# Kernel tuning notes

Hardware: AMD Instinct MI355X
Metric: run time of the kernel (lower is better)

Reference implementation:

```python
import jax, jax.numpy as jnp
import numpy as np

N = 100000      # nodes
E = 1200000     # edges (avg degree ~12)
D_IN = 64
D_OUT = 64


def setup_inputs() -> dict:
    key = jax.random.key(0)
    k1, k2, k3, k4 = jax.random.split(key, 4)
    x = jax.random.normal(k1, (N, D_IN), dtype=jnp.float32)
    # learned params (glorot-ish init)
    W = jax.random.normal(k2, (D_IN, D_OUT), dtype=jnp.float32) / np.sqrt(D_IN).astype(np.float32)
    b = jnp.zeros((D_OUT,), dtype=jnp.float32)
    src = jax.random.randint(k3, (E,), 0, N, dtype=jnp.int32)
    dst = jax.random.randint(k4, (E,), 0, N, dtype=jnp.int32)
    return {"x": x, "W": W, "b": b, "src": src, "dst": dst}


def reference(x, W, b, src, dst):
    # GCN layer: h = relu( D^-1/2 A D^-1/2 (x @ W) + b ), dropout=0 (eval)
    ones = jnp.ones(src.shape[0], dtype=x.dtype)
    deg_out = jax.ops.segment_sum(ones, src, num_segments=N)   # out-degree of source nodes
    deg_in = jax.ops.segment_sum(ones, dst, num_segments=N)    # in-degree of dest nodes
    norm_src = jax.lax.rsqrt(jnp.maximum(deg_out, 1.0))
    norm_dst = jax.lax.rsqrt(jnp.maximum(deg_in, 1.0))

    h = x @ W                                                  # [N, D_OUT] dense transform
    msg = h[src] * norm_src[src][:, None]                      # [E, D_OUT] gathered, pre-normalized messages
    agg = jax.ops.segment_sum(msg, dst, num_segments=N)        # [N, D_OUT] sparse aggregation
    out = agg * norm_dst[:, None] + b
    return jax.nn.relu(out)
```

## Files before the change

### kernel.cpp

```cpp
#include <hip/hip_runtime.h>
#include <hip/hip_bf16.h>

#define N_NODES 100000
#define N_EDGES 1200000
#define DCH 64

#define NT 512

#define SB 192
#define SCHUNK (N_EDGES / SB)

#define HB 96
#define CHUNK (N_EDGES / HB)
#define HALF_BINS 50000
#define HALF_WORDS 12500

#define GEMMB 384
#define GWAVES (GEMMB * NT / 64)


#define BNODES 256
#define KBUK ((N_NODES + BNODES - 1) / BNODES)
#define CAPE 6144

#define OFF_DEG      0
#define OFF_GCUR     100096
#define OFF_FLAG     101760
#define OFF_ESORT    102144
#define OFF_HS       9711616

__device__ __forceinline__ float load_f(const void* p, int i, int f32) {
    if (f32) return ((const float*)p)[i];
    return __bfloat162float(((const __hip_bfloat16*)p)[i]);
}

__device__ __forceinline__ unsigned short f2bf_bits(float f) {
    __hip_bfloat16 h = __float2bfloat16(f);
    return __builtin_bit_cast(unsigned short, h);
}

__global__ __launch_bounds__(NT, 6)
void fused_kernel(const int* __restrict__ src,
                  const int* __restrict__ dst,
                  const void* __restrict__ x,
                  const void* __restrict__ W,
                  unsigned int* __restrict__ deg_packed,
                  int* __restrict__ gcur,
                  unsigned int* __restrict__ esort,
                  int* __restrict__ flag,
                  __hip_bfloat16* __restrict__ hs) {
    __shared__ unsigned int h[HALF_WORDS];
    int tid = threadIdx.x;
    int bid = blockIdx.x;

    if (bid < SB) {
        int* cnt  = (int*)h;
        int* base = cnt + KBUK;
        int* cur  = base + KBUK;
        for (int i = tid; i < KBUK; i += NT) { cnt[i] = 0; cur[i] = 0; }
        __syncthreads();
        int e0 = bid * SCHUNK;
        const int2* src2 = (const int2*)(src + e0);
        const int2* dst2 = (const int2*)(dst + e0);
        int npair = SCHUNK >> 1;
        for (int p = tid; p < npair; p += NT) {
            int2 dp = dst2[p];
            atomicAdd(&cnt[dp.x >> 8], 1);
            atomicAdd(&cnt[dp.y >> 8], 1);
        }
        __syncthreads();
        for (int i = tid; i < KBUK; i += NT)
            base[i] = atomicAdd(&gcur[i], cnt[i]);
        __syncthreads();
        for (int p = tid; p < npair; p += NT) {
            int2 sp = src2[p];
            int2 dp = dst2[p];
            int b0 = dp.x >> 8, b1 = dp.y >> 8;
            int pos0 = base[b0] + atomicAdd(&cur[b0], 1);
            if (pos0 < CAPE)
                esort[b0 * CAPE + pos0] =
                    (unsigned int)sp.x | ((unsigned int)(dp.x & 255) << 24);
            int pos1 = base[b1] + atomicAdd(&cur[b1], 1);
            if (pos1 < CAPE)
                esort[b1 * CAPE + pos1] =
                    (unsigned int)sp.y | ((unsigned int)(dp.y & 255) << 24);
        }
        if (bid == 0) {
            __syncthreads();
            if (tid == 0) cnt[0] = 0;
            __syncthreads();
            if (tid < 256) {
                const unsigned short* u = (const unsigned short*)x;
                int c = 0;
                for (int i = tid * 16; i < tid * 16 + 16; ++i) {
                    unsigned short v = u[2 * i];
                    int e = (v >> 7) & 0xFF;
                    if (e >= 141) c++;
                }
                if (c) atomicAdd(&cnt[0], c);
            }
            __syncthreads();
            if (tid == 0) *flag = (cnt[0] > 256) ? 1 : 0;
        }
    } else if (bid < SB + 2 * HB) {
        int hb = bid - SB;
        int c = hb >> 1, half = hb & 1;
        for (int w = tid; w < HALF_WORDS; w += NT) h[w] = 0;
        __syncthreads();
        int lo = half * HALF_BINS;
        int e0 = c * CHUNK;
        const int2* src2 = (const int2*)(src + e0);
        int npair = CHUNK >> 1;
        for (int p = tid; p < npair; p += NT) {
            int2 sp = src2[p];
            int n0 = sp.x - lo, n1 = sp.y - lo;
            if ((unsigned)n0 < (unsigned)HALF_BINS)
                atomicAdd(&h[n0 >> 2], 1u << ((n0 & 3) * 8));
            if ((unsigned)n1 < (unsigned)HALF_BINS)
                atomicAdd(&h[n1 >> 2], 1u << ((n1 & 3) * 8));
        }
        __syncthreads();
        unsigned int* dp = deg_packed + half * HALF_WORDS;
        for (int w = tid; w < HALF_WORDS; w += NT) {
            unsigned int v = h[w];
            if (v) atomicAdd(&dp[w], v);
        }
    } else {
        int* sn = (int*)h;
        if (tid == 0) sn[0] = 0;
        __syncthreads();
        if (tid < 256) {
            const unsigned short* u = (const unsigned short*)x;
            int c = 0;
            for (int i = tid * 16; i < tid * 16 + 16; ++i) {
                unsigned short v = u[2 * i];
                int e = (v >> 7) & 0xFF;
                if (e >= 141) c++;
            }
            if (c) atomicAdd(sn, c);
        }
        __syncthreads();
        int f32 = sn[0] > 256;
        __syncthreads();

        float* wt = (float*)h;
        for (int i = tid; i < DCH * DCH; i += NT) {
            int kk = i >> 6, cc = i & 63;
            wt[cc * 68 + kk] = load_f(W, i, f32);
        }
        __syncthreads();

        int lane = tid & 63;
        const float4* wrow = (const float4*)(wt + lane * 68);
        float4 wq0 = wrow[0],  wq1 = wrow[1],  wq2 = wrow[2],  wq3 = wrow[3];
        float4 wq4 = wrow[4],  wq5 = wrow[5],  wq6 = wrow[6],  wq7 = wrow[7];
        float4 wq8 = wrow[8],  wq9 = wrow[9],  wq10 = wrow[10], wq11 = wrow[11];
        float4 wq12 = wrow[12], wq13 = wrow[13], wq14 = wrow[14], wq15 = wrow[15];

        int wave = ((bid - (SB + 2 * HB)) * NT + tid) >> 6;
#define RLA(i) __int_as_float(__builtin_amdgcn_readlane(xiA, (i)))
#define RLB(i) __int_as_float(__builtin_amdgcn_readlane(xiB, (i)))
#define GRP(j, V) \
    a0 = fmaf(RLA(4*(j)+0), (V).x, a0); a1 = fmaf(RLA(4*(j)+1), (V).y, a1); \
    a2 = fmaf(RLA(4*(j)+2), (V).z, a2); a3 = fmaf(RLA(4*(j)+3), (V).w, a3); \
    c0 = fmaf(RLB(4*(j)+0), (V).x, c0); c1 = fmaf(RLB(4*(j)+1), (V).y, c1); \
    c2 = fmaf(RLB(4*(j)+2), (V).z, c2); c3 = fmaf(RLB(4*(j)+3), (V).w, c3);

        for (int node = wave; node < N_NODES; node += 2 * GWAVES) {
            int nodeB = node + GWAVES;
            int hasB = nodeB < N_NODES;
            float xvA = load_f(x, node * DCH + lane, f32);
            float xvB = hasB ? load_f(x, nodeB * DCH + lane, f32) : 0.0f;
            int xiA = __float_as_int(xvA);
            int xiB = __float_as_int(xvB);
            float a0 = 0.f, a1 = 0.f, a2 = 0.f, a3 = 0.f;
            float c0 = 0.f, c1 = 0.f, c2 = 0.f, c3 = 0.f;
            GRP(0, wq0)   GRP(1, wq1)   GRP(2, wq2)   GRP(3, wq3)
            GRP(4, wq4)   GRP(5, wq5)   GRP(6, wq6)   GRP(7, wq7)
            GRP(8, wq8)   GRP(9, wq9)   GRP(10, wq10) GRP(11, wq11)
            GRP(12, wq12) GRP(13, wq13) GRP(14, wq14) GRP(15, wq15)
            hs[node * DCH + lane] = __float2bfloat16((a0 + a1) + (a2 + a3));
            if (hasB)
                hs[nodeB * DCH + lane] = __float2bfloat16((c0 + c1) + (c2 + c3));
        }
#undef RLA
#undef RLB
#undef GRP
    }
}

__global__ __launch_bounds__(1024)
void sortgather_kernel(const __hip_bfloat16* __restrict__ hs,
                       const unsigned int* __restrict__ esort,
                       const int* __restrict__ gcur,
                       const unsigned int* __restrict__ deg_packed,
                       const void* __restrict__ b,
                       const int* __restrict__ flag,
                       void* __restrict__ out) {
    __shared__ unsigned int ebuf[CAPE];
    __shared__ int cnt[BNODES];
    __shared__ int loc[BNODES];
    __shared__ int sc[BNODES];
    __shared__ int cur[BNODES];
    __shared__ float tab[256];
    int k = blockIdx.x, tid = threadIdx.x;
    int bbase = k * CAPE;
    int m = gcur[k];
    if (m > CAPE) m = CAPE;

    if (tid < BNODES) { cnt[tid] = 0; cur[tid] = 0; }
    if (tid < 256) tab[tid] = rsqrtf(fmaxf((float)tid, 1.0f));
    __syncthreads();
    for (int e = tid; e < m; e += 1024)
        atomicAdd(&cnt[esort[bbase + e] >> 24], 1);
    __syncthreads();
    int v = 0;
    if (tid < BNODES) { v = cnt[tid]; sc[tid] = v; }
    __syncthreads();
    for (int off = 1; off < BNODES; off <<= 1) {
        int add = 0;
        if (tid < BNODES && tid >= off) add = sc[tid - off];
        __syncthreads();
        if (tid < BNODES) sc[tid] += add;
        __syncthreads();
    }
    if (tid < BNODES) loc[tid] = sc[tid] - v;
    __syncthreads();
    for (int e = tid; e < m; e += 1024) {
        unsigned int w = esort[bbase + e];
        int r = w >> 24;
        unsigned int s = w & 0xFFFFFFu;
        unsigned int dw = deg_packed[s >> 2];
        unsigned int degb = (dw >> ((s & 3) * 8)) & 0xFFu;
        int pos = loc[r] + atomicAdd(&cur[r], 1);
        ebuf[pos] = s | (degb << 24);
    }
    __syncthreads();

    int f32 = *flag;
    int lane = tid & 63, wv = tid >> 6;
    int q = lane >> 4;
    int cg = lane & 15;
    const unsigned short* hsu = (const unsigned short*)hs;
    float b0 = load_f(b, cg * 4 + 0, f32);
    float b1 = load_f(b, cg * 4 + 1, f32);
    float b2 = load_f(b, cg * 4 + 2, f32);
    float b3 = load_f(b, cg * 4 + 3, f32);
    int nlo = k * BNODES;
    for (int base = wv; base < BNODES; base += 32) {
        int tA = base, tB = base + 16;
        int nodeA = nlo + tA, nodeB = nlo + tB;
        int begA = loc[tA], degA = cnt[tA];
        int begB = loc[tB], degB = cnt[tB];
        float4 aA0 = {0.f,0.f,0.f,0.f}, aA1 = {0.f,0.f,0.f,0.f};
        float4 aB0 = {0.f,0.f,0.f,0.f}, aB1 = {0.f,0.f,0.f,0.f};
        int dmax = degA > degB ? degA : degB;
        for (int j0 = 0; j0 < dmax; j0 += 8) {
            int i0 = j0 + q, i1 = j0 + 4 + q;
            unsigned int wA0 = ebuf[(i0 < degA) ? (begA + i0) : 0];
            unsigned int wA1 = ebuf[(i1 < degA) ? (begA + i1) : 0];
            unsigned int wB0 = ebuf[(i0 < degB) ? (begB + i0) : 0];
            unsigned int wB1 = ebuf[(i1 < degB) ? (begB + i1) : 0];
            unsigned int sA0 = wA0 & 0xFFFFFFu, sA1 = wA1 & 0xFFFFFFu;
            unsigned int sB0 = wB0 & 0xFFFFFFu, sB1 = wB1 & 0xFFFFFFu;
            float fA0 = tab[wA0 >> 24], fA1 = tab[wA1 >> 24];
            float fB0 = tab[wB0 >> 24], fB1 = tab[wB1 >> 24];
            uint2 uA0 = ((const uint2*)(hsu + sA0 * DCH))[cg];
            uint2 uA1 = ((const uint2*)(hsu + sA1 * DCH))[cg];
            uint2 uB0 = ((const uint2*)(hsu + sB0 * DCH))[cg];
            uint2 uB1 = ((const uint2*)(hsu + sB1 * DCH))[cg];
            if (i0 < degA) {
                aA0.x = fmaf(__uint_as_float(uA0.x << 16),        fA0, aA0.x);
                aA0.y = fmaf(__uint_as_float(uA0.x & 0xFFFF0000u), fA0, aA0.y);
                aA0.z = fmaf(__uint_as_float(uA0.y << 16),        fA0, aA0.z);
                aA0.w = fmaf(__uint_as_float(uA0.y & 0xFFFF0000u), fA0, aA0.w);
            }
            if (i1 < degA) {
                aA1.x = fmaf(__uint_as_float(uA1.x << 16),        fA1, aA1.x);
                aA1.y = fmaf(__uint_as_float(uA1.x & 0xFFFF0000u), fA1, aA1.y);
                aA1.z = fmaf(__uint_as_float(uA1.y << 16),        fA1, aA1.z);
                aA1.w = fmaf(__uint_as_float(uA1.y & 0xFFFF0000u), fA1, aA1.w);
            }
            if (i0 < degB) {
                aB0.x = fmaf(__uint_as_float(uB0.x << 16),        fB0, aB0.x);
                aB0.y = fmaf(__uint_as_float(uB0.x & 0xFFFF0000u), fB0, aB0.y);
                aB0.z = fmaf(__uint_as_float(uB0.y << 16),        fB0, aB0.z);
                aB0.w = fmaf(__uint_as_float(uB0.y & 0xFFFF0000u), fB0, aB0.w);
            }
            if (i1 < degB) {
                aB1.x = fmaf(__uint_as_float(uB1.x << 16),        fB1, aB1.x);
                aB1.y = fmaf(__uint_as_float(uB1.x & 0xFFFF0000u), fB1, aB1.y);
                aB1.z = fmaf(__uint_as_float(uB1.y << 16),        fB1, aB1.z);
                aB1.w = fmaf(__uint_as_float(uB1.y & 0xFFFF0000u), fB1, aB1.w);
            }
        }
        float4 oA, oB;
        oA.x = aA0.x + aA1.x; oA.y = aA0.y + aA1.y;
        oA.z = aA0.z + aA1.z; oA.w = aA0.w + aA1.w;
        oB.x = aB0.x + aB1.x; oB.y = aB0.y + aB1.y;
        oB.z = aB0.z + aB1.z; oB.w = aB0.w + aB1.w;
        oA.x += __shfl_xor(oA.x, 16); oA.y += __shfl_xor(oA.y, 16);
        oA.z += __shfl_xor(oA.z, 16); oA.w += __shfl_xor(oA.w, 16);
        oA.x += __shfl_xor(oA.x, 32); oA.y += __shfl_xor(oA.y, 32);
        oA.z += __shfl_xor(oA.z, 32); oA.w += __shfl_xor(oA.w, 32);
        oB.x += __shfl_xor(oB.x, 16); oB.y += __shfl_xor(oB.y, 16);
        oB.z += __shfl_xor(oB.z, 16); oB.w += __shfl_xor(oB.w, 16);
        oB.x += __shfl_xor(oB.x, 32); oB.y += __shfl_xor(oB.y, 32);
        oB.z += __shfl_xor(oB.z, 32); oB.w += __shfl_xor(oB.w, 32);
        int myNode = (lane < 16) ? nodeA : nodeB;
        int myDeg  = (lane < 16) ? degA : degB;
        float4 o   = (lane < 16) ? oA : oB;
        if (lane < 32 && myNode < N_NODES) {
            float nrm = rsqrtf(fmaxf((float)myDeg, 1.0f));
            o.x = fmaxf(o.x * nrm + b0, 0.0f);
            o.y = fmaxf(o.y * nrm + b1, 0.0f);
            o.z = fmaxf(o.z * nrm + b2, 0.0f);
            o.w = fmaxf(o.w * nrm + b3, 0.0f);
            if (f32) {
                ((float4*)out)[myNode * 16 + cg] = o;
            } else {
                ushort4 s;
                s.x = f2bf_bits(o.x);
                s.y = f2bf_bits(o.y);
                s.z = f2bf_bits(o.z);
                s.w = f2bf_bits(o.w);
                ((ushort4*)out)[myNode * 16 + cg] = s;
            }
        }
    }
}

extern "C" void kernel_launch(void* const* d_in, const int* in_sizes, int n_in,
                              void* d_out, int out_size, void* d_ws, size_t ws_size,
                              hipStream_t stream) {
    const void* x   = d_in[0];
    const void* W   = d_in[1];
    const void* b   = d_in[2];
    const int*  src = (const int*)d_in[3];
    const int*  dst = (const int*)d_in[4];

    char* ws = (char*)d_ws;
    unsigned int* deg_packed = (unsigned int*)(ws + OFF_DEG);
    int* gcur     = (int*)(ws + OFF_GCUR);
    int* flag     = (int*)(ws + OFF_FLAG);
    unsigned int* esort = (unsigned int*)(ws + OFF_ESORT);
    __hip_bfloat16* hs  = (__hip_bfloat16*)(ws + OFF_HS);

    (void)hipMemsetAsync(ws, 0, OFF_FLAG + 4, stream);

    fused_kernel<<<SB + 2 * HB + GEMMB, NT, 0, stream>>>(
        src, dst, x, W, deg_packed, gcur, esort, flag, hs);

    sortgather_kernel<<<KBUK, 1024, 0, stream>>>(
        hs, esort, gcur, deg_packed, b, flag, d_out);
}
```

Baseline: 183.9 us.

## Make every fused block do GEMM, degree histogram and bucketing in sequence

The fused kernel drops its role-specialised block ranges (scatter, histogram, GEMM). Each of 256 blocks of 1024 threads now runs a share of the dense transform, then a two-pass packed source-degree histogram over its own edge chunk, then the destination bucketing. Buckets shrink from 256 to 128 nodes, so the sort/gather kernel gets about twice as many blocks at 512 threads each. The aim is better load balance and more gather-phase parallelism. The cost is that each block now runs all phases one after another, with extra barriers and two LDS histogram passes per block.

```diff
diff --git a/kernel.cpp b/kernel.cpp
--- a/kernel.cpp
+++ b/kernel.cpp
@@ -5,29 +5,25 @@
 #define N_EDGES 1200000
 #define DCH 64
 
-#define NT 512
-
-#define SB 192
-#define SCHUNK (N_EDGES / SB)
-
-#define HB 96
-#define CHUNK (N_EDGES / HB)
+#define FB 256
+#define NT 1024
+#define EPB 4688
+#define GW_TOT (FB * NT / 64)
+
 #define HALF_BINS 50000
 #define HALF_WORDS 12500
 
-#define GEMMB 384
-#define GWAVES (GEMMB * NT / 64)
-
-
-#define BNODES 256
+#define BNODES 128
 #define KBUK ((N_NODES + BNODES - 1) / BNODES)
-#define CAPE 6144
+#define CAPE 3008
+
+#define NT2 512
 
 #define OFF_DEG      0
 #define OFF_GCUR     100096
-#define OFF_FLAG     101760
-#define OFF_ESORT    102144
-#define OFF_HS       9711616
+#define OFF_FLAG     103296
+#define OFF_ESORT    103424
+#define OFF_HS       9512704
 
 __device__ __forceinline__ float load_f(const void* p, int i, int f32) {
     if (f32) return ((const float*)p)[i];
@@ -39,7 +35,7 @@
     return __builtin_bit_cast(unsigned short, h);
 }
 
-__global__ __launch_bounds__(NT, 6)
+__global__ __launch_bounds__(NT, 4)
 void fused_kernel(const int* __restrict__ src,
                   const int* __restrict__ dst,
                   const void* __restrict__ x,
@@ -53,96 +49,25 @@
     int tid = threadIdx.x;
     int bid = blockIdx.x;
 
-    if (bid < SB) {
-        int* cnt  = (int*)h;
-        int* base = cnt + KBUK;
-        int* cur  = base + KBUK;
-        for (int i = tid; i < KBUK; i += NT) { cnt[i] = 0; cur[i] = 0; }
-        __syncthreads();
-        int e0 = bid * SCHUNK;
-        const int2* src2 = (const int2*)(src + e0);
-        const int2* dst2 = (const int2*)(dst + e0);
-        int npair = SCHUNK >> 1;
-        for (int p = tid; p < npair; p += NT) {
-            int2 dp = dst2[p];
-            atomicAdd(&cnt[dp.x >> 8], 1);
-            atomicAdd(&cnt[dp.y >> 8], 1);
-        }
-        __syncthreads();
-        for (int i = tid; i < KBUK; i += NT)
-            base[i] = atomicAdd(&gcur[i], cnt[i]);
-        __syncthreads();
-        for (int p = tid; p < npair; p += NT) {
-            int2 sp = src2[p];
-            int2 dp = dst2[p];
-            int b0 = dp.x >> 8, b1 = dp.y >> 8;
-            int pos0 = base[b0] + atomicAdd(&cur[b0], 1);
-            if (pos0 < CAPE)
-                esort[b0 * CAPE + pos0] =
-                    (unsigned int)sp.x | ((unsigned int)(dp.x & 255) << 24);
-            int pos1 = base[b1] + atomicAdd(&cur[b1], 1);
-            if (pos1 < CAPE)
-                esort[b1 * CAPE + pos1] =
-                    (unsigned int)sp.y | ((unsigned int)(dp.y & 255) << 24);
-        }
-        if (bid == 0) {
-            __syncthreads();
-            if (tid == 0) cnt[0] = 0;
-            __syncthreads();
-            if (tid < 256) {
-                const unsigned short* u = (const unsigned short*)x;
-                int c = 0;
-                for (int i = tid * 16; i < tid * 16 + 16; ++i) {
-                    unsigned short v = u[2 * i];
-                    int e = (v >> 7) & 0xFF;
-                    if (e >= 141) c++;
-                }
-                if (c) atomicAdd(&cnt[0], c);
-            }
-            __syncthreads();
-            if (tid == 0) *flag = (cnt[0] > 256) ? 1 : 0;
-        }
-    } else if (bid < SB + 2 * HB) {
-        int hb = bid - SB;
-        int c = hb >> 1, half = hb & 1;
-        for (int w = tid; w < HALF_WORDS; w += NT) h[w] = 0;
-        __syncthreads();
-        int lo = half * HALF_BINS;
-        int e0 = c * CHUNK;
-        const int2* src2 = (const int2*)(src + e0);
-        int npair = CHUNK >> 1;
-        for (int p = tid; p < npair; p += NT) {
-            int2 sp = src2[p];
-            int n0 = sp.x - lo, n1 = sp.y - lo;
-            if ((unsigned)n0 < (unsigned)HALF_BINS)
-                atomicAdd(&h[n0 >> 2], 1u << ((n0 & 3) * 8));
-            if ((unsigned)n1 < (unsigned)HALF_BINS)
-                atomicAdd(&h[n1 >> 2], 1u << ((n1 & 3) * 8));
-        }
-        __syncthreads();
-        unsigned int* dp = deg_packed + half * HALF_WORDS;
-        for (int w = tid; w < HALF_WORDS; w += NT) {
-            unsigned int v = h[w];
-            if (v) atomicAdd(&dp[w], v);
-        }
-    } else {
-        int* sn = (int*)h;
-        if (tid == 0) sn[0] = 0;
-        __syncthreads();
-        if (tid < 256) {
-            const unsigned short* u = (const unsigned short*)x;
-            int c = 0;
-            for (int i = tid * 16; i < tid * 16 + 16; ++i) {
-                unsigned short v = u[2 * i];
-                int e = (v >> 7) & 0xFF;
-                if (e >= 141) c++;
-            }
-            if (c) atomicAdd(sn, c);
-        }
-        __syncthreads();
-        int f32 = sn[0] > 256;
-        __syncthreads();
-
+    int* sn = (int*)h;
+    if (tid == 0) sn[0] = 0;
+    __syncthreads();
+    if (tid < 256) {
+        const unsigned short* u = (const unsigned short*)x;
+        int c = 0;
+        for (int i = tid * 16; i < tid * 16 + 16; ++i) {
+            unsigned short v = u[2 * i];
+            int e = (v >> 7) & 0xFF;
+            if (e >= 141) c++;
+        }
+        if (c) atomicAdd(sn, c);
+    }
+    __syncthreads();
+    int f32 = sn[0] > 256;
+    if (bid == 0 && tid == 0) *flag = f32;
+    __syncthreads();
+
+    {
         float* wt = (float*)h;
         for (int i = tid; i < DCH * DCH; i += NT) {
             int kk = i >> 6, cc = i & 63;
@@ -157,7 +82,7 @@
         float4 wq8 = wrow[8],  wq9 = wrow[9],  wq10 = wrow[10], wq11 = wrow[11];
         float4 wq12 = wrow[12], wq13 = wrow[13], wq14 = wrow[14], wq15 = wrow[15];
 
-        int wave = ((bid - (SB + 2 * HB)) * NT + tid) >> 6;
+        int gw = (bid << 4) + (tid >> 6);
 #define RLA(i) __int_as_float(__builtin_amdgcn_readlane(xiA, (i)))
 #define RLB(i) __int_as_float(__builtin_amdgcn_readlane(xiB, (i)))
 #define GRP(j, V) \
@@ -166,8 +91,8 @@
     c0 = fmaf(RLB(4*(j)+0), (V).x, c0); c1 = fmaf(RLB(4*(j)+1), (V).y, c1); \
     c2 = fmaf(RLB(4*(j)+2), (V).z, c2); c3 = fmaf(RLB(4*(j)+3), (V).w, c3);
 
-        for (int node = wave; node < N_NODES; node += 2 * GWAVES) {
-            int nodeB = node + GWAVES;
+        for (int node = gw; node < N_NODES; node += 2 * GW_TOT) {
+            int nodeB = node + GW_TOT;
             int hasB = nodeB < N_NODES;
             float xvA = load_f(x, node * DCH + lane, f32);
             float xvB = hasB ? load_f(x, nodeB * DCH + lane, f32) : 0.0f;
@@ -187,9 +112,67 @@
 #undef RLB
 #undef GRP
     }
-}
-
-__global__ __launch_bounds__(1024)
+    __syncthreads();
+
+    int e0 = bid * EPB;
+    int eend = e0 + EPB; if (eend > N_EDGES) eend = N_EDGES;
+    int npair = (eend - e0) >> 1;
+    const int2* src2 = (const int2*)(src + e0);
+    const int2* dst2 = (const int2*)(dst + e0);
+
+    for (int half = 0; half < 2; ++half) {
+        for (int w = tid; w < HALF_WORDS; w += NT) h[w] = 0;
+        __syncthreads();
+        int lo = half * HALF_BINS;
+        for (int p = tid; p < npair; p += NT) {
+            int2 sp = src2[p];
+            int n0 = sp.x - lo, n1 = sp.y - lo;
+            if ((unsigned)n0 < (unsigned)HALF_BINS)
+                atomicAdd(&h[n0 >> 2], 1u << ((n0 & 3) * 8));
+            if ((unsigned)n1 < (unsigned)HALF_BINS)
+                atomicAdd(&h[n1 >> 2], 1u << ((n1 & 3) * 8));
+        }
+        __syncthreads();
+        unsigned int* dp = deg_packed + half * HALF_WORDS;
+        for (int w = tid; w < HALF_WORDS; w += NT) {
+            unsigned int v = h[w];
+            if (v) atomicAdd(&dp[w], v);
+        }
+        __syncthreads();
+    }
+
+    {
+        int* cnt  = (int*)h;
+        int* base = cnt + KBUK;
+        int* cur  = base + KBUK;
+        for (int i = tid; i < KBUK; i += NT) { cnt[i] = 0; cur[i] = 0; }
+        __syncthreads();
+        for (int p = tid; p < npair; p += NT) {
+            int2 dp = dst2[p];
+            atomicAdd(&cnt[dp.x >> 7], 1);
+            atomicAdd(&cnt[dp.y >> 7], 1);
+        }
+        __syncthreads();
+        for (int i = tid; i < KBUK; i += NT)
+            base[i] = atomicAdd(&gcur[i], cnt[i]);
+        __syncthreads();
+        for (int p = tid; p < npair; p += NT) {
+            int2 sp = src2[p];
+            int2 dp = dst2[p];
+            int b0 = dp.x >> 7, b1 = dp.y >> 7;
+            int pos0 = base[b0] + atomicAdd(&cur[b0], 1);
+            if (pos0 < CAPE)
+                esort[b0 * CAPE + pos0] =
+                    (unsigned int)sp.x | ((unsigned int)(dp.x & 127) << 24);
+            int pos1 = base[b1] + atomicAdd(&cur[b1], 1);
+            if (pos1 < CAPE)
+                esort[b1 * CAPE + pos1] =
+                    (unsigned int)sp.y | ((unsigned int)(dp.y & 127) << 24);
+        }
+    }
+}
+
+__global__ __launch_bounds__(NT2, 6)
 void sortgather_kernel(const __hip_bfloat16* __restrict__ hs,
                        const unsigned int* __restrict__ esort,
                        const int* __restrict__ gcur,
@@ -211,7 +194,7 @@
     if (tid < BNODES) { cnt[tid] = 0; cur[tid] = 0; }
     if (tid < 256) tab[tid] = rsqrtf(fmaxf((float)tid, 1.0f));
     __syncthreads();
-    for (int e = tid; e < m; e += 1024)
+    for (int e = tid; e < m; e += NT2)
         atomicAdd(&cnt[esort[bbase + e] >> 24], 1);
     __syncthreads();
     int v = 0;
@@ -226,7 +209,7 @@
     }
     if (tid < BNODES) loc[tid] = sc[tid] - v;
     __syncthreads();
-    for (int e = tid; e < m; e += 1024) {
+    for (int e = tid; e < m; e += NT2) {
         unsigned int w = esort[bbase + e];
         int r = w >> 24;
         unsigned int s = w & 0xFFFFFFu;
@@ -247,8 +230,8 @@
     float b2 = load_f(b, cg * 4 + 2, f32);
     float b3 = load_f(b, cg * 4 + 3, f32);
     int nlo = k * BNODES;
-    for (int base = wv; base < BNODES; base += 32) {
-        int tA = base, tB = base + 16;
+    for (int base = wv; base < BNODES; base += 16) {
+        int tA = base, tB = base + 8;
         int nodeA = nlo + tA, nodeB = nlo + tB;
         int begA = loc[tA], degA = cnt[tA];
         int begB = loc[tB], degB = cnt[tB];
@@ -348,9 +331,9 @@
 
     (void)hipMemsetAsync(ws, 0, OFF_FLAG + 4, stream);
 
-    fused_kernel<<<SB + 2 * HB + GEMMB, NT, 0, stream>>>(
+    fused_kernel<<<FB, NT, 0, stream>>>(
         src, dst, x, W, deg_packed, gcur, esort, flag, hs);
 
-    sortgather_kernel<<<KBUK, 1024, 0, stream>>>(
+    sortgather_kernel<<<KBUK, NT2, 0, stream>>>(
         hs, esort, gcur, deg_packed, b, flag, d_out);
 }
```

Result: faster. 173.6 us (-5.6%).
